# Kernel optimization log

Measured on AMD Instinct MI355X. Metric: run time of the kernel, lower is better.

The kernel has to match this reference:

```python
import jax, jax.numpy as jnp
import numpy as np

NUM_CLASSES = 2
THRESHOLD = 0.35
NEGPOS_RATIO = 3
VAR0, VAR1 = 0.1, 0.2
ALPHA = 1.0
B, P, G = 16, 131072, 64


def _iou(a, b):
    # a: [G,4] point-form gts, b: [P,4] point-form priors -> [G,P]
    tl = jnp.maximum(a[:, None, :2], b[None, :, :2])
    br = jnp.minimum(a[:, None, 2:], b[None, :, 2:])
    wh = jnp.clip(br - tl, 0.0)
    inter = wh[..., 0] * wh[..., 1]
    area_a = (a[:, 2] - a[:, 0]) * (a[:, 3] - a[:, 1])
    area_b = (b[:, 2] - b[:, 0]) * (b[:, 3] - b[:, 1])
    return inter / (area_a[:, None] + area_b[None, :] - inter)


def setup_inputs() -> dict:
    key = jax.random.key(0)
    k1, k2, k3, k4, k5, k6 = jax.random.split(key, 6)
    loc_preds = jax.random.normal(k1, (B, P, 4), jnp.float32)
    cls_preds = jax.random.normal(k2, (B, P, NUM_CLASSES), jnp.float32)
    # priors in center form [cx, cy, w, h]
    pcxy = jax.random.uniform(k3, (P, 2), jnp.float32)
    pwh = 0.02 + 0.15 * jax.random.uniform(k4, (P, 2), jnp.float32)
    priorbox = jnp.concatenate([pcxy, pwh], axis=1)
    # ground-truth boxes; stored as [y1,x1,y2,x2,label] so that the module's
    # column permutation [1,0,3,2] yields valid point-form [x1,y1,x2,y2]
    xy1 = 0.8 * jax.random.uniform(k5, (B, G, 2), jnp.float32)
    wh = 0.02 + 0.1 * jax.random.uniform(k6, (B, G, 2), jnp.float32)
    xy2 = xy1 + wh
    boxes_perm = jnp.stack([xy1[..., 1], xy1[..., 0], xy2[..., 1], xy2[..., 0]], axis=-1)
    labels = jnp.ones((B, G, 1), jnp.float32)  # single foreground class (face)
    targets = jnp.concatenate([boxes_perm, labels], axis=-1)
    return {"loc_preds": loc_preds, "cls_preds": cls_preds,
            "priorbox": priorbox, "targets": targets}


def _loss(loc_preds, cls_preds, priorbox, targets):
    priors_c = priorbox[: loc_preds.shape[1], :]
    priors_pt = jnp.concatenate(
        [priors_c[:, :2] - priors_c[:, 2:] / 2,
         priors_c[:, :2] + priors_c[:, 2:] / 2], axis=1)
    num_g = targets.shape[1]

    def match_one(t):
        gts = t[:, :4][:, jnp.array([1, 0, 3, 2])]  # -> point form [x1,y1,x2,y2]
        labels = t[:, 4]
        ov = _iou(gts, priors_pt)                    # [G,P]
        best_prior_idx = jnp.argmax(ov, axis=1)      # [G]
        bto = jnp.max(ov, axis=0)                    # [P] best gt overlap per prior
        bti = jnp.argmax(ov, axis=0)                 # [P]
        bto = bto.at[best_prior_idx].set(2.0)        # force best prior per gt
        bti = bti.at[best_prior_idx].set(jnp.arange(num_g))
        conf = jnp.where(bto < THRESHOLD, 0.0, labels[bti])
        m = gts[bti]                                 # [P,4] matched gt boxes
        g_cxcy = ((m[:, :2] + m[:, 2:]) / 2 - priors_c[:, :2]) / (VAR0 * priors_c[:, 2:])
        g_wh = jnp.log((m[:, 2:] - m[:, :2]) / priors_c[:, 2:]) / VAR1
        return conf, jnp.concatenate([g_cxcy, g_wh], axis=1)

    cls_batch, loc_batch = jax.vmap(match_one)(targets)
    cls_batch = jax.lax.stop_gradient(cls_batch)   # targets require no grad
    loc_batch = jax.lax.stop_gradient(loc_batch)

    pos = cls_batch > 0                              # [B,P]
    npos = jnp.sum(pos)

    # smooth-L1 over positive priors, mean over selected elements (size_average)
    d = loc_preds - loc_batch
    ad = jnp.abs(d)
    sl1 = jnp.where(ad < 1.0, 0.5 * d * d, ad - 0.5)
    loss_loc = jnp.sum(sl1 * pos[..., None]) / jnp.maximum(npos * 4, 1).astype(sl1.dtype)

    # per-prior CE loss for hard-negative mining
    ignore = cls_batch < 0
    lbl = jnp.where(ignore, 0.0, cls_batch).astype(jnp.int32)
    lse = jax.nn.logsumexp(cls_preds, axis=-1)       # [B,P]
    gathered = jnp.take_along_axis(cls_preds, lbl[..., None], axis=-1)[..., 0]
    loss_c = jnp.where(pos | ignore, 0.0, lse - gathered)
    # two-stage sort: rank of each prior by descending loss
    loss_idx = jnp.argsort(-loss_c, axis=1)
    idx_rank = jnp.argsort(loss_idx, axis=1)
    num_pos_img = jnp.sum(pos, axis=1, keepdims=True)
    num_neg = jnp.minimum(NEGPOS_RATIO * num_pos_img, pos.shape[1] - 1)
    neg = idx_rank < num_neg
    mask = pos | neg
    # cross-entropy over mined samples, mean over selected (size_average)
    loss_cls = jnp.sum((lse - gathered) * mask) / jnp.maximum(jnp.sum(mask), 1).astype(lse.dtype)

    loss = (loss_cls + ALPHA * loss_loc) / npos.astype(lse.dtype)
    return loss, loss_loc, loss_cls


def reference(loc_preds, cls_preds, priorbox, targets):
    return _loss(loc_preds, cls_preds, priorbox, targets)
```

## Files before the change

### kernel.cpp

```cpp
#include <hip/hip_runtime.h>

#define BB 16
#define PP 131072
#define GG 64
#define THRESH 0.35f
#define EXPL 0.086f
#define EXPS 0.0495f
#define CLSB 0.049f
#define NCELL 32
#define NCHM 64
#define CPM 2048
#define NCHL 64
#define CPL 2048
#define NCC 64
#define CPC 2048

#define OFF_BESTP   0
#define OFF_H1TOT   524288
#define OFF_NPOSP   786432
#define OFF_PCP     790528
#define OFF_LOCP    794624
#define OFF_CIDX    798720
#define OFF_NEGS    798784
#define OFF_DONE    798848
#define OFF_RESN    798912
#define OFF_RESK    798976
#define OFF_RESC    799040
#define OFF_RESL    799104
#define OFF_PU8     799168
#define OFF_KEYS    2896320
#define OFF_CAND    11284928

__global__ __launch_bounds__(256) void k_match(
    const float* __restrict__ priorbox, const float* __restrict__ targets,
    unsigned long long* __restrict__ bestp, unsigned char* __restrict__ pu8,
    unsigned* __restrict__ h1tot, unsigned* __restrict__ cidx,
    float* __restrict__ negs, unsigned* __restrict__ done)
{
    __shared__ unsigned mskS[2 * NCELL * NCELL];
    __shared__ unsigned mskL[2 * NCELL * NCELL];
    __shared__ float4 gxy[GG];
    __shared__ unsigned long long sbest[GG];
    const int b = blockIdx.y, chunk = blockIdx.x, tid = threadIdx.x;

    if (tid < 64) h1tot[b * 4096 + chunk * 64 + tid] = 0u;
    if (chunk == 0 && tid == 0) { cidx[b] = 0u; negs[b] = 0.f; if (b == 0) *done = 0u; }
    for (int i = tid; i < 2 * NCELL * NCELL; i += 256) { mskS[i] = 0u; mskL[i] = 0u; }
    if (tid < GG) {
        const float* t = targets + (size_t)(b * GG + tid) * 5;
        gxy[tid] = make_float4(t[1], t[0], t[3], t[2]);
        sbest[tid] = 0ull;
    }
    __syncthreads();

    {
        const int g = tid & 63, strip = tid >> 6;
        float4 a = gxy[g];
        unsigned bit = 1u << (g & 31);
        const int word = g >> 5;
        {
            int cx0 = max(0, (int)((a.x - EXPS) * (float)NCELL));
            int cx1 = min(NCELL - 1, (int)ceilf((a.z + EXPS) * (float)NCELL) - 1);
            int cy0 = max(0, (int)((a.y - EXPS) * (float)NCELL));
            int cy1 = min(NCELL - 1, (int)ceilf((a.w + EXPS) * (float)NCELL) - 1);
            for (int cy = cy0 + strip; cy <= cy1; cy += 4)
                for (int cx = cx0; cx <= cx1; cx++)
                    atomicOr(&mskS[2 * (cy * NCELL + cx) + word], bit);
        }
        {
            int cx0 = max(0, (int)((a.x - EXPL) * (float)NCELL));
            int cx1 = min(NCELL - 1, (int)ceilf((a.z + EXPL) * (float)NCELL) - 1);
            int cy0 = max(0, (int)((a.y - EXPL) * (float)NCELL));
            int cy1 = min(NCELL - 1, (int)ceilf((a.w + EXPL) * (float)NCELL) - 1);
            for (int cy = cy0 + strip; cy <= cy1; cy += 4)
                for (int cx = cx0; cx <= cx1; cx++)
                    atomicOr(&mskL[2 * (cy * NCELL + cx) + word], bit);
        }
    }
    __syncthreads();

#pragma unroll
    for (int j = 0; j < 8; j++) {
        const int p = chunk * CPM + j * 256 + tid;
        float4 pr = *reinterpret_cast<const float4*>(priorbox + (size_t)p * 4);
        float hx = 0.5f * pr.z, hy = 0.5f * pr.w;
        float px1 = pr.x - hx, py1 = pr.y - hy;
        float px2 = pr.x + hx, py2 = pr.y + hy;
        float par = (px2 - px1) * (py2 - py1);
        int cx = min(NCELL - 1, max(0, (int)(pr.x * (float)NCELL)));
        int cy = min(NCELL - 1, max(0, (int)(pr.y * (float)NCELL)));
        const unsigned* mb = (fmaxf(hx, hy) <= CLSB) ? mskS : mskL;
        uint2 mm = *reinterpret_cast<const uint2*>(&mb[2 * (cy * NCELL + cx)]);
        unsigned long long m = ((unsigned long long)mm.y << 32) | mm.x;
        const unsigned long long notp = (unsigned long long)(~(unsigned)p);
        float bv = -1.f; int bg = 0;
        while (m) {
            const int g0 = __ffsll(m) - 1; m &= m - 1;
            const bool has1 = (m != 0ull);
            const int g1 = has1 ? (__ffsll(m) - 1) : g0;
            if (has1) m &= m - 1;
            float4 a0 = gxy[g0];
            float4 a1 = gxy[g1];
            float w0 = fmaxf(fminf(a0.z, px2) - fmaxf(a0.x, px1), 0.f);
            float h0 = fmaxf(fminf(a0.w, py2) - fmaxf(a0.y, py1), 0.f);
            float w1 = fmaxf(fminf(a1.z, px2) - fmaxf(a1.x, px1), 0.f);
            float h1 = fmaxf(fminf(a1.w, py2) - fmaxf(a1.y, py1), 0.f);
            float ar0 = (a0.z - a0.x) * (a0.w - a0.y);
            float ar1 = (a1.z - a1.x) * (a1.w - a1.y);
            float i0 = w0 * h0, i1 = w1 * h1;
            float v0 = i0 * __builtin_amdgcn_rcpf(ar0 + par - i0);
            float v1 = i1 * __builtin_amdgcn_rcpf(ar1 + par - i1);
            if (v0 > bv) { bv = v0; bg = g0; }
            if (has1 && v1 > bv) { bv = v1; bg = g1; }
            if (v0 > 0.f)
                atomicMax(&sbest[g0],
                          (((unsigned long long)__float_as_uint(v0)) << 32) | notp);
            if (has1 && v1 > 0.f)
                atomicMax(&sbest[g1],
                          (((unsigned long long)__float_as_uint(v1)) << 32) | notp);
        }
        pu8[(size_t)b * PP + p] = (unsigned char)(bg | ((bv >= THRESH) ? 0x80 : 0));
    }

    __syncthreads();
    if (tid < GG) bestp[(b * NCHM + chunk) * GG + tid] = sbest[tid];
}

__global__ __launch_bounds__(256) void k_loss(
    const float* __restrict__ loc_preds, const float* __restrict__ cls_preds,
    const float* __restrict__ priorbox, const float* __restrict__ targets,
    const unsigned long long* __restrict__ bestp, const unsigned char* __restrict__ pu8,
    unsigned* __restrict__ keys, unsigned* __restrict__ h1tot,
    int* __restrict__ nposp, float* __restrict__ pcp, float* __restrict__ locp)
{
    __shared__ unsigned hcnt[4096];
    __shared__ unsigned ovr[CPL];
    __shared__ float4 gxy[GG];
    __shared__ float glab[GG];
    __shared__ float sred[8];
    __shared__ int sredi[4];
    const int b = blockIdx.y, chunk = blockIdx.x, tid = threadIdx.x;
    const int lane = tid & 63, wid = tid >> 6;

    for (int i = tid; i < 4096; i += 256) hcnt[i] = 0u;
    for (int i = tid; i < CPL; i += 256) ovr[i] = 0u;
    if (tid < GG) {
        const float* t = targets + (size_t)(b * GG + tid) * 5;
        gxy[tid] = make_float4(t[1], t[0], t[3], t[2]);
        glab[tid] = t[4];
    }
    __syncthreads();
    if (tid < GG) {
        unsigned long long m = 0ull;
#pragma unroll 8
        for (int c = 0; c < NCHM; c++) {
            unsigned long long v = bestp[(b * NCHM + c) * GG + tid];
            m = v > m ? v : m;
        }
        if (m) {
            unsigned p = ~((unsigned)(m & 0xFFFFFFFFull));
            if ((int)(p >> 11) == chunk)
                atomicMax(&ovr[p & (CPL - 1)], (unsigned)tid + 1u);
        }
    }
    __syncthreads();

    float locpart = 0.f, clspart = 0.f; int cnt = 0;
#pragma unroll
    for (int j = 0; j < 8; j++) {
        const int plocal = j * 256 + tid;
        const size_t ip = (size_t)b * PP + chunk * CPL + plocal;
        const unsigned m8 = pu8[ip];
        int g = m8 & 63;
        bool pos = (m8 >> 7) != 0;
        const unsigned o = ovr[plocal];
        if (o) { pos = true; g = (int)o - 1; }
        const float2 cl = *reinterpret_cast<const float2*>(cls_preds + ip * 2);
        const float mx = fmaxf(cl.x, cl.y);
        const float lse = mx + log1pf(expf(fminf(cl.x, cl.y) - mx));
        unsigned key = 0u;
        if (pos && glab[g] > 0.f) {
            float gathered = (((int)glab[g]) == 0) ? cl.x : cl.y;
            clspart += lse - gathered;
            cnt++;
            const int p = chunk * CPL + plocal;
            float4 pr = *reinterpret_cast<const float4*>(priorbox + (size_t)p * 4);
            float4 gt = gxy[g];
            float gcx = ((gt.x + gt.z) * 0.5f - pr.x) / (0.1f * pr.z);
            float gcy = ((gt.y + gt.w) * 0.5f - pr.y) / (0.1f * pr.w);
            float gw = logf((gt.z - gt.x) / pr.z) / 0.2f;
            float gh = logf((gt.w - gt.y) / pr.w) / 0.2f;
            float4 lp = *reinterpret_cast<const float4*>(loc_preds + ip * 4);
            float d0 = lp.x - gcx, d1 = lp.y - gcy, d2 = lp.z - gw, d3 = lp.w - gh;
            float a0 = fabsf(d0), a1 = fabsf(d1), a2 = fabsf(d2), a3 = fabsf(d3);
            locpart += ((a0 < 1.f) ? 0.5f * d0 * d0 : a0 - 0.5f)
                     + ((a1 < 1.f) ? 0.5f * d1 * d1 : a1 - 0.5f)
                     + ((a2 < 1.f) ? 0.5f * d2 * d2 : a2 - 0.5f)
                     + ((a3 < 1.f) ? 0.5f * d3 * d3 : a3 - 0.5f);
        } else {
            float lc = lse - cl.x;
            key = __float_as_uint(lc);
            atomicAdd(&hcnt[key >> 20], 1u);
        }
        keys[ip] = key;
    }

    for (int o = 32; o; o >>= 1) {
        locpart += __shfl_xor(locpart, o);
        clspart += __shfl_xor(clspart, o);
        cnt     += __shfl_xor(cnt, o);
    }
    if (lane == 0) { sred[wid] = locpart; sred[4 + wid] = clspart; sredi[wid] = cnt; }
    __syncthreads();
    if (tid == 0) {
        float l = sred[0] + sred[1] + sred[2] + sred[3];
        float c = sred[4] + sred[5] + sred[6] + sred[7];
        int n = sredi[0] + sredi[1] + sredi[2] + sredi[3];
        nposp[b * NCHL + chunk] = n;
        pcp[b * NCHL + chunk] = c;
        locp[b * NCHL + chunk] = l;
    }
    __syncthreads();
    for (int i = tid; i < 4096; i += 256) {
        unsigned cc = hcnt[i];
        if (cc) atomicAdd(&h1tot[b * 4096 + i], cc);
    }
}

template <int NBINS>
__device__ void find_kth_par(const unsigned* __restrict__ h, int k, int* sel, int* krem)
{
    constexpr int PER = NBINS / 256;
    __shared__ unsigned wsum_[4];
    __shared__ int res_[2];
    const int tid = threadIdx.x, lane = tid & 63, wid = tid >> 6;
    __syncthreads();
    unsigned s = 0;
#pragma unroll
    for (int i = 0; i < PER; i++) s += h[NBINS - 1 - (tid * PER + i)];
    unsigned incl = s;
    for (int d = 1; d < 64; d <<= 1) {
        unsigned t = __shfl_up(incl, d);
        if (lane >= d) incl += t;
    }
    if (lane == 63) wsum_[wid] = incl;
    if (tid == 0) { res_[0] = -1; res_[1] = 0; }
    __syncthreads();
    unsigned woff = 0;
    for (int w = 0; w < 4; w++) woff += (w < wid) ? wsum_[w] : 0u;
    const unsigned texcl = woff + incl - s;
    if (k > 0 && texcl < (unsigned)k && texcl + s >= (unsigned)k) {
        unsigned run = texcl;
        for (int i = 0; i < PER; i++) {
            unsigned hv = h[NBINS - 1 - (tid * PER + i)];
            run += hv;
            if (run >= (unsigned)k) {
                res_[0] = NBINS - 1 - (tid * PER + i);
                res_[1] = k - (int)(run - hv);
                break;
            }
        }
    }
    __syncthreads();
    *sel = res_[0]; *krem = res_[1];
}

__device__ float block_sum_f(float v)
{
    __shared__ float rs[4];
    const int tid = threadIdx.x;
    __syncthreads();
    for (int o = 32; o; o >>= 1) v += __shfl_xor(v, o);
    if ((tid & 63) == 0) rs[tid >> 6] = v;
    __syncthreads();
    return rs[0] + rs[1] + rs[2] + rs[3];
}

__device__ int np_of_image(const int* __restrict__ nposp, int b)
{
    __shared__ int snp;
    const int tid = threadIdx.x;
    int v = (tid < 64) ? nposp[b * NCHL + tid] : 0;
    if (tid < 64) {
        for (int o = 32; o; o >>= 1) v += __shfl_xor(v, o);
        if (tid == 0) snp = v;
    }
    __syncthreads();
    return snp;
}

__global__ __launch_bounds__(256) void k_compact(
    const unsigned* __restrict__ keys, const unsigned* __restrict__ h1tot,
    const int* __restrict__ nposp, unsigned* __restrict__ cand,
    unsigned* __restrict__ cidx, float* __restrict__ negs)
{
    __shared__ unsigned wcnt[4], wbase[4];
    __shared__ unsigned bbase;
    const int b = blockIdx.y, chunk = blockIdx.x, tid = threadIdx.x;
    const int lane = tid & 63, wid = tid >> 6;

    unsigned kv[8];
#pragma unroll
    for (int j = 0; j < 8; j++)
        kv[j] = keys[(size_t)b * PP + chunk * CPC + j * 256 + tid];

    const int np = np_of_image(nposp, b);
    const int k = min(3 * np, PP - 1);
    int sel1, kk1;
    find_kth_par<4096>(h1tot + b * 4096, k, &sel1, &kk1);
    const unsigned s1 = (unsigned)sel1;

    float nv = 0.f;
    if (sel1 >= 0) {
#pragma unroll
        for (int j = 0; j < 8; j++)
            if ((kv[j] >> 20) > s1) nv += __uint_as_float(kv[j]);
    }
    float nsum = block_sum_f(nv);
    if (tid == 0 && nsum != 0.f) atomicAdd(&negs[b], nsum);

    unsigned long long mv[8];
    unsigned wn = 0;
#pragma unroll
    for (int j = 0; j < 8; j++) {
        mv[j] = __ballot((kv[j] >> 20) == s1);
        wn += (unsigned)__popcll(mv[j]);
    }
    if (lane == 0) wcnt[wid] = wn;
    __syncthreads();
    if (tid == 0) {
        unsigned run = 0;
        for (int w = 0; w < 4; w++) { wbase[w] = run; run += wcnt[w]; }
        bbase = run ? atomicAdd(&cidx[b], run) : 0u;
    }
    __syncthreads();
    unsigned run = bbase + wbase[wid];
    const unsigned long long lanemask = (1ull << lane) - 1ull;
#pragma unroll
    for (int j = 0; j < 8; j++) {
        if ((kv[j] >> 20) == s1)
            cand[(size_t)b * PP + run + (unsigned)__popcll(mv[j] & lanemask)] = kv[j];
        run += (unsigned)__popcll(mv[j]);
    }
}

__global__ __launch_bounds__(256) void k_select(
    const unsigned* __restrict__ cand, const unsigned* __restrict__ cidx,
    const unsigned* __restrict__ h1tot, const int* __restrict__ nposp,
    const float* __restrict__ pcp, const float* __restrict__ locp,
    const float* __restrict__ negs,
    int* __restrict__ resn, int* __restrict__ resk,
    float* __restrict__ resc, float* __restrict__ resl,
    unsigned* __restrict__ done, float* __restrict__ out)
{
    __shared__ unsigned ch[1024];
    __shared__ float cs[1024];
    __shared__ int lastflag;
    const int b = blockIdx.x, tid = threadIdx.x;

    const int np = np_of_image(nposp, b);
    const int k = min(3 * np, PP - 1);
    int sel1, kk1;
    find_kth_par<4096>(h1tot + b * 4096, k, &sel1, &kk1);
    const unsigned ncand = cidx[b];

    float pv = (tid < 64) ? pcp[b * NCHL + tid] : 0.f;
    float lv = (tid < 64) ? locp[b * NCHL + tid] : 0.f;
    float pcsum = block_sum_f(pv);
    float locsum = block_sum_f(lv);

    for (int i = tid; i < 1024; i += 256) { ch[i] = 0u; cs[i] = 0.f; }
    __syncthreads();
    for (unsigned i = tid; i < ncand; i += 256) {
        unsigned v = cand[(size_t)b * PP + i];
        unsigned bin = (v >> 10) & 1023u;
        atomicAdd(&ch[bin], 1u);
        atomicAdd(&cs[bin], __uint_as_float(v));
    }
    __syncthreads();
    int sel2, kk2;
    find_kth_par<1024>(ch, (sel1 < 0) ? 0 : kk1, &sel2, &kk2);
    float s2v = 0.f;
    for (int i = tid * 4; i < tid * 4 + 4; i++)
        if (sel2 >= 0 && i > sel2) s2v += cs[i];
    float sumhi2 = block_sum_f(s2v);

    __syncthreads();
    for (int i = tid; i < 1024; i += 256) { ch[i] = 0u; cs[i] = 0.f; }
    __syncthreads();
    if (sel2 >= 0) {
        for (unsigned i = tid; i < ncand; i += 256) {
            unsigned v = cand[(size_t)b * PP + i];
            if (((v >> 10) & 1023u) == (unsigned)sel2) {
                atomicAdd(&ch[v & 1023u], 1u);
                atomicAdd(&cs[v & 1023u], __uint_as_float(v));
            }
        }
    }
    __syncthreads();
    int sel3, needeq;
    find_kth_par<1024>(ch, (sel2 < 0) ? 0 : kk2, &sel3, &needeq);
    float s3v = 0.f;
    for (int i = tid * 4; i < tid * 4 + 4; i++)
        if (sel3 >= 0 && i > sel3) s3v += cs[i];
    float sumhi3 = block_sum_f(s3v);

    if (tid == 0) {
        float add = 0.f;
        if (sel3 >= 0 && needeq > 0) {
            unsigned Kstar = ((unsigned)sel1 << 20) | ((unsigned)sel2 << 10) | (unsigned)sel3;
            add = needeq * __uint_as_float(Kstar);
        }
        resn[b] = np;
        resk[b] = k;
        resc[b] = pcsum + negs[b] + sumhi2 + sumhi3 + add;
        resl[b] = locsum;
        __threadfence();
        lastflag = (atomicAdd(done, 1u) == BB - 1) ? 1 : 0;
    }
    __syncthreads();
    if (!lastflag) return;
    if (tid == 0) __threadfence();
    __syncthreads();

    int n = 0, kk = 0; float c = 0.f, l = 0.f;
    if (tid < BB) { n = resn[tid]; kk = resk[tid]; c = resc[tid]; l = resl[tid]; }
    if (tid < 64) {
        for (int o = 8; o; o >>= 1) {
            n += __shfl_xor(n, o); kk += __shfl_xor(kk, o);
            c += __shfl_xor(c, o); l += __shfl_xor(l, o);
        }
    }
    if (tid == 0) {
        long long maskc = (long long)n + kk;
        float denom_loc = (float)((4 * n > 1) ? 4 * n : 1);
        float denom_cls = (float)((maskc > 1) ? maskc : 1);
        float loss_loc = l / denom_loc;
        float loss_cls = c / denom_cls;
        out[0] = (loss_cls + loss_loc) / (float)n;
        out[1] = loss_loc;
        out[2] = loss_cls;
    }
}

extern "C" void kernel_launch(void* const* d_in, const int* in_sizes, int n_in,
                              void* d_out, int out_size, void* d_ws, size_t ws_size,
                              hipStream_t stream)
{
    const float* loc_preds = (const float*)d_in[0];
    const float* cls_preds = (const float*)d_in[1];
    const float* priorbox  = (const float*)d_in[2];
    const float* targets   = (const float*)d_in[3];
    float* out = (float*)d_out;

    char* ws = (char*)d_ws;
    unsigned long long* bestp = (unsigned long long*)(ws + OFF_BESTP);
    unsigned* h1tot = (unsigned*)(ws + OFF_H1TOT);
    int*      nposp = (int*)(ws + OFF_NPOSP);
    float*    pcp   = (float*)(ws + OFF_PCP);
    float*    locp  = (float*)(ws + OFF_LOCP);
    unsigned* cidx  = (unsigned*)(ws + OFF_CIDX);
    float*    negs  = (float*)(ws + OFF_NEGS);
    unsigned* done  = (unsigned*)(ws + OFF_DONE);
    int*      resn  = (int*)(ws + OFF_RESN);
    int*      resk  = (int*)(ws + OFF_RESK);
    float*    resc  = (float*)(ws + OFF_RESC);
    float*    resl  = (float*)(ws + OFF_RESL);
    unsigned char* pu8 = (unsigned char*)(ws + OFF_PU8);
    unsigned* keys  = (unsigned*)(ws + OFF_KEYS);
    unsigned* cand  = (unsigned*)(ws + OFF_CAND);

    k_match<<<dim3(NCHM, BB), 256, 0, stream>>>(priorbox, targets, bestp, pu8,
                                                h1tot, cidx, negs, done);
    k_loss<<<dim3(NCHL, BB), 256, 0, stream>>>(loc_preds, cls_preds, priorbox, targets,
                                               bestp, pu8, keys, h1tot,
                                               nposp, pcp, locp);
    k_compact<<<dim3(NCC, BB), 256, 0, stream>>>(keys, h1tot, nposp, cand, cidx, negs);
    k_select<<<BB, 256, 0, stream>>>(cand, cidx, h1tot, nposp, pcp, locp, negs,
                                     resn, resk, resc, resl, done, out);
}
```

Measured before the change: 99.50 us.

## Fuse matching and loss kernels, patch forced-match priors in a small fix kernel

Merges the prior-matching pass and the per-prior loss/key pass into one kernel. Each block now computes loss contributions right after matching, using the threshold-based assignment. The per-gt forced best-prior overrides are applied afterwards by a tiny k_fix kernel, which adjusts keys, histogram counts and partial sums incrementally. A separate zeroing kernel replaces the in-kernel initialization. This removes one full pass over pu8/priorbox and a kernel launch, at the cost of extra correction logic that must exactly reproduce the override semantics.

```diff
diff --git a/kernel.cpp b/kernel.cpp
--- a/kernel.cpp
+++ b/kernel.cpp
@@ -8,10 +8,8 @@
 #define EXPS 0.0495f
 #define CLSB 0.049f
 #define NCELL 32
-#define NCHM 64
-#define CPM 2048
-#define NCHL 64
-#define CPL 2048
+#define NCH 64
+#define CPR 2048
 #define NCC 64
 #define CPC 2048
 
@@ -31,24 +29,42 @@
 #define OFF_KEYS    2896320
 #define OFF_CAND    11284928
 
-__global__ __launch_bounds__(256) void k_match(
-    const float* __restrict__ priorbox, const float* __restrict__ targets,
-    unsigned long long* __restrict__ bestp, unsigned char* __restrict__ pu8,
+__global__ __launch_bounds__(256) void k_zero(
     unsigned* __restrict__ h1tot, unsigned* __restrict__ cidx,
     float* __restrict__ negs, unsigned* __restrict__ done)
 {
+    const int gid = blockIdx.x * 256 + threadIdx.x;
+    h1tot[gid] = 0u;
+    if (blockIdx.x == 0) {
+        if (threadIdx.x < BB) { cidx[threadIdx.x] = 0u; negs[threadIdx.x] = 0.f; }
+        if (threadIdx.x == BB) *done = 0u;
+    }
+}
+
+__global__ __launch_bounds__(256) void k_matchloss(
+    const float* __restrict__ priorbox, const float* __restrict__ targets,
+    const float* __restrict__ loc_preds, const float* __restrict__ cls_preds,
+    unsigned long long* __restrict__ bestp, unsigned char* __restrict__ pu8,
+    unsigned* __restrict__ keys, unsigned* __restrict__ h1tot,
+    int* __restrict__ nposp, float* __restrict__ pcp, float* __restrict__ locp)
+{
     __shared__ unsigned mskS[2 * NCELL * NCELL];
     __shared__ unsigned mskL[2 * NCELL * NCELL];
+    __shared__ unsigned hcnt[4096];
     __shared__ float4 gxy[GG];
+    __shared__ float glab[GG];
     __shared__ unsigned long long sbest[GG];
+    __shared__ float sred[8];
+    __shared__ int sredi[4];
     const int b = blockIdx.y, chunk = blockIdx.x, tid = threadIdx.x;
-
-    if (tid < 64) h1tot[b * 4096 + chunk * 64 + tid] = 0u;
-    if (chunk == 0 && tid == 0) { cidx[b] = 0u; negs[b] = 0.f; if (b == 0) *done = 0u; }
+    const int lane = tid & 63, wid = tid >> 6;
+
     for (int i = tid; i < 2 * NCELL * NCELL; i += 256) { mskS[i] = 0u; mskL[i] = 0u; }
+    for (int i = tid; i < 4096; i += 256) hcnt[i] = 0u;
     if (tid < GG) {
         const float* t = targets + (size_t)(b * GG + tid) * 5;
         gxy[tid] = make_float4(t[1], t[0], t[3], t[2]);
+        glab[tid] = t[4];
         sbest[tid] = 0ull;
     }
     __syncthreads();
@@ -79,9 +95,11 @@
     }
     __syncthreads();
 
+    float locpart = 0.f, clspart = 0.f; int cnt = 0;
 #pragma unroll
     for (int j = 0; j < 8; j++) {
-        const int p = chunk * CPM + j * 256 + tid;
+        const int p = chunk * CPR + j * 256 + tid;
+        const size_t ip = (size_t)b * PP + p;
         float4 pr = *reinterpret_cast<const float4*>(priorbox + (size_t)p * 4);
         float hx = 0.5f * pr.z, hy = 0.5f * pr.w;
         float px1 = pr.x - hx, py1 = pr.y - hy;
@@ -119,73 +137,18 @@
                 atomicMax(&sbest[g1],
                           (((unsigned long long)__float_as_uint(v1)) << 32) | notp);
         }
-        pu8[(size_t)b * PP + p] = (unsigned char)(bg | ((bv >= THRESH) ? 0x80 : 0));
-    }
-
-    __syncthreads();
-    if (tid < GG) bestp[(b * NCHM + chunk) * GG + tid] = sbest[tid];
-}
-
-__global__ __launch_bounds__(256) void k_loss(
-    const float* __restrict__ loc_preds, const float* __restrict__ cls_preds,
-    const float* __restrict__ priorbox, const float* __restrict__ targets,
-    const unsigned long long* __restrict__ bestp, const unsigned char* __restrict__ pu8,
-    unsigned* __restrict__ keys, unsigned* __restrict__ h1tot,
-    int* __restrict__ nposp, float* __restrict__ pcp, float* __restrict__ locp)
-{
-    __shared__ unsigned hcnt[4096];
-    __shared__ unsigned ovr[CPL];
-    __shared__ float4 gxy[GG];
-    __shared__ float glab[GG];
-    __shared__ float sred[8];
-    __shared__ int sredi[4];
-    const int b = blockIdx.y, chunk = blockIdx.x, tid = threadIdx.x;
-    const int lane = tid & 63, wid = tid >> 6;
-
-    for (int i = tid; i < 4096; i += 256) hcnt[i] = 0u;
-    for (int i = tid; i < CPL; i += 256) ovr[i] = 0u;
-    if (tid < GG) {
-        const float* t = targets + (size_t)(b * GG + tid) * 5;
-        gxy[tid] = make_float4(t[1], t[0], t[3], t[2]);
-        glab[tid] = t[4];
-    }
-    __syncthreads();
-    if (tid < GG) {
-        unsigned long long m = 0ull;
-#pragma unroll 8
-        for (int c = 0; c < NCHM; c++) {
-            unsigned long long v = bestp[(b * NCHM + c) * GG + tid];
-            m = v > m ? v : m;
-        }
-        if (m) {
-            unsigned p = ~((unsigned)(m & 0xFFFFFFFFull));
-            if ((int)(p >> 11) == chunk)
-                atomicMax(&ovr[p & (CPL - 1)], (unsigned)tid + 1u);
-        }
-    }
-    __syncthreads();
-
-    float locpart = 0.f, clspart = 0.f; int cnt = 0;
-#pragma unroll
-    for (int j = 0; j < 8; j++) {
-        const int plocal = j * 256 + tid;
-        const size_t ip = (size_t)b * PP + chunk * CPL + plocal;
-        const unsigned m8 = pu8[ip];
-        int g = m8 & 63;
-        bool pos = (m8 >> 7) != 0;
-        const unsigned o = ovr[plocal];
-        if (o) { pos = true; g = (int)o - 1; }
+        const bool posbit = (bv >= THRESH);
+        pu8[ip] = (unsigned char)(bg | (posbit ? 0x80 : 0));
+
         const float2 cl = *reinterpret_cast<const float2*>(cls_preds + ip * 2);
         const float mx = fmaxf(cl.x, cl.y);
         const float lse = mx + log1pf(expf(fminf(cl.x, cl.y) - mx));
         unsigned key = 0u;
-        if (pos && glab[g] > 0.f) {
-            float gathered = (((int)glab[g]) == 0) ? cl.x : cl.y;
+        if (posbit && glab[bg] > 0.f) {
+            float gathered = (((int)glab[bg]) == 0) ? cl.x : cl.y;
             clspart += lse - gathered;
             cnt++;
-            const int p = chunk * CPL + plocal;
-            float4 pr = *reinterpret_cast<const float4*>(priorbox + (size_t)p * 4);
-            float4 gt = gxy[g];
+            float4 gt = gxy[bg];
             float gcx = ((gt.x + gt.z) * 0.5f - pr.x) / (0.1f * pr.z);
             float gcy = ((gt.y + gt.w) * 0.5f - pr.y) / (0.1f * pr.w);
             float gw = logf((gt.z - gt.x) / pr.z) / 0.2f;
@@ -213,17 +176,111 @@
     if (lane == 0) { sred[wid] = locpart; sred[4 + wid] = clspart; sredi[wid] = cnt; }
     __syncthreads();
     if (tid == 0) {
-        float l = sred[0] + sred[1] + sred[2] + sred[3];
-        float c = sred[4] + sred[5] + sred[6] + sred[7];
-        int n = sredi[0] + sredi[1] + sredi[2] + sredi[3];
-        nposp[b * NCHL + chunk] = n;
-        pcp[b * NCHL + chunk] = c;
-        locp[b * NCHL + chunk] = l;
-    }
+        nposp[b * NCH + chunk] = sredi[0] + sredi[1] + sredi[2] + sredi[3];
+        pcp[b * NCH + chunk] = sred[4] + sred[5] + sred[6] + sred[7];
+        locp[b * NCH + chunk] = sred[0] + sred[1] + sred[2] + sred[3];
+    }
+    if (tid < GG) bestp[(b * NCH + chunk) * GG + tid] = sbest[tid];
     __syncthreads();
     for (int i = tid; i < 4096; i += 256) {
         unsigned cc = hcnt[i];
         if (cc) atomicAdd(&h1tot[b * 4096 + i], cc);
+    }
+}
+
+__global__ void k_fix(
+    const float* __restrict__ priorbox, const float* __restrict__ targets,
+    const float* __restrict__ loc_preds, const float* __restrict__ cls_preds,
+    const unsigned long long* __restrict__ bestp, const unsigned char* __restrict__ pu8,
+    unsigned* __restrict__ keys, unsigned* __restrict__ h1tot,
+    int* __restrict__ nposp, float* __restrict__ pcp, float* __restrict__ locp)
+{
+    __shared__ unsigned sp[GG];
+    const int b = blockIdx.x, g = threadIdx.x;
+
+    unsigned long long m = 0ull;
+#pragma unroll 8
+    for (int c = 0; c < NCH; c++) {
+        unsigned long long v = bestp[(b * NCH + c) * GG + g];
+        m = v > m ? v : m;
+    }
+    sp[g] = m ? ~((unsigned)(m & 0xFFFFFFFFull)) : 0xFFFFFFFFu;
+    __syncthreads();
+
+    bool winner = (sp[g] != 0xFFFFFFFFu);
+    if (winner)
+        for (int g2 = g + 1; g2 < GG; g2++)
+            if (sp[g2] == sp[g]) { winner = false; break; }
+
+    int dn = 0; float dpc = 0.f, dloc = 0.f;
+    if (winner) {
+        const unsigned p = sp[g];
+        const size_t ip = (size_t)b * PP + p;
+        const unsigned m8 = pu8[ip];
+        const int oldg = m8 & 63;
+        const bool oldposbit = (m8 >> 7) != 0;
+        const float labg = targets[(size_t)(b * GG + g) * 5 + 4];
+        const float labold = targets[(size_t)(b * GG + oldg) * 5 + 4];
+        const bool counted_old = oldposbit && (labold > 0.f);
+        const bool counted_new = (labg > 0.f);
+        const float2 cl = *reinterpret_cast<const float2*>(cls_preds + ip * 2);
+        const float mx = fmaxf(cl.x, cl.y);
+        const float lse = mx + log1pf(expf(fminf(cl.x, cl.y) - mx));
+        float4 pr = *reinterpret_cast<const float4*>(priorbox + (size_t)p * 4);
+        float4 lp = *reinterpret_cast<const float4*>(loc_preds + ip * 4);
+
+#define SL1(GT)                                                             \
+        ({                                                                  \
+            const float* t_ = targets + (size_t)(b * GG + (GT)) * 5;        \
+            float x1 = t_[1], y1 = t_[0], x2 = t_[3], y2 = t_[2];           \
+            float gcx = ((x1 + x2) * 0.5f - pr.x) / (0.1f * pr.z);          \
+            float gcy = ((y1 + y2) * 0.5f - pr.y) / (0.1f * pr.w);          \
+            float gw = logf((x2 - x1) / pr.z) / 0.2f;                       \
+            float gh = logf((y2 - y1) / pr.w) / 0.2f;                       \
+            float d0 = lp.x - gcx, d1 = lp.y - gcy, d2 = lp.z - gw,         \
+                  d3 = lp.w - gh;                                           \
+            float a0 = fabsf(d0), a1 = fabsf(d1), a2 = fabsf(d2),           \
+                  a3 = fabsf(d3);                                           \
+            ((a0 < 1.f) ? 0.5f * d0 * d0 : a0 - 0.5f) +                     \
+            ((a1 < 1.f) ? 0.5f * d1 * d1 : a1 - 0.5f) +                     \
+            ((a2 < 1.f) ? 0.5f * d2 * d2 : a2 - 0.5f) +                     \
+            ((a3 < 1.f) ? 0.5f * d3 * d3 : a3 - 0.5f);                      \
+        })
+
+        if (counted_new) {
+            float gathered = (((int)labg) == 0) ? cl.x : cl.y;
+            if (!counted_old) {
+                unsigned okey = keys[ip];
+                if (okey) atomicSub(&h1tot[b * 4096 + (okey >> 20)], 1u);
+                keys[ip] = 0u;
+                dn = 1; dpc = lse - gathered; dloc = SL1(g);
+            } else {
+                float gathold = (((int)labold) == 0) ? cl.x : cl.y;
+                dpc = gathold - gathered;
+                dloc = SL1(g) - SL1(oldg);
+            }
+        } else {
+            if (counted_old) {
+                float gathold = (((int)labold) == 0) ? cl.x : cl.y;
+                dn = -1; dpc = -(lse - gathold); dloc = -SL1(oldg);
+                float lc = lse - cl.x;
+                unsigned nk = __float_as_uint(lc);
+                keys[ip] = nk;
+                atomicAdd(&h1tot[b * 4096 + (nk >> 20)], 1u);
+            }
+        }
+#undef SL1
+    }
+
+    for (int o = 32; o; o >>= 1) {
+        dn += __shfl_xor(dn, o);
+        dpc += __shfl_xor(dpc, o);
+        dloc += __shfl_xor(dloc, o);
+    }
+    if (g == 0) {
+        if (dn)         atomicAdd(&nposp[b * NCH], dn);
+        if (dpc != 0.f) atomicAdd(&pcp[b * NCH], dpc);
+        if (dloc != 0.f) atomicAdd(&locp[b * NCH], dloc);
     }
 }
 
@@ -280,7 +337,7 @@
 {
     __shared__ int snp;
     const int tid = threadIdx.x;
-    int v = (tid < 64) ? nposp[b * NCHL + tid] : 0;
+    int v = (tid < 64) ? nposp[b * NCH + tid] : 0;
     if (tid < 64) {
         for (int o = 32; o; o >>= 1) v += __shfl_xor(v, o);
         if (tid == 0) snp = v;
@@ -364,8 +421,8 @@
     find_kth_par<4096>(h1tot + b * 4096, k, &sel1, &kk1);
     const unsigned ncand = cidx[b];
 
-    float pv = (tid < 64) ? pcp[b * NCHL + tid] : 0.f;
-    float lv = (tid < 64) ? locp[b * NCHL + tid] : 0.f;
+    float pv = (tid < 64) ? pcp[b * NCH + tid] : 0.f;
+    float lv = (tid < 64) ? locp[b * NCH + tid] : 0.f;
     float pcsum = block_sum_f(pv);
     float locsum = block_sum_f(lv);
 
@@ -470,11 +527,12 @@
     unsigned* keys  = (unsigned*)(ws + OFF_KEYS);
     unsigned* cand  = (unsigned*)(ws + OFF_CAND);
 
-    k_match<<<dim3(NCHM, BB), 256, 0, stream>>>(priorbox, targets, bestp, pu8,
-                                                h1tot, cidx, negs, done);
-    k_loss<<<dim3(NCHL, BB), 256, 0, stream>>>(loc_preds, cls_preds, priorbox, targets,
-                                               bestp, pu8, keys, h1tot,
-                                               nposp, pcp, locp);
+    k_zero<<<256, 256, 0, stream>>>(h1tot, cidx, negs, done);
+    k_matchloss<<<dim3(NCH, BB), 256, 0, stream>>>(priorbox, targets, loc_preds,
+                                                   cls_preds, bestp, pu8, keys, h1tot,
+                                                   nposp, pcp, locp);
+    k_fix<<<BB, 64, 0, stream>>>(priorbox, targets, loc_preds, cls_preds,
+                                 bestp, pu8, keys, h1tot, nposp, pcp, locp);
     k_compact<<<dim3(NCC, BB), 256, 0, stream>>>(keys, h1tot, nposp, cand, cidx, negs);
     k_select<<<BB, 256, 0, stream>>>(cand, cidx, h1tot, nposp, pcp, locp, negs,
                                      resn, resk, resc, resl, done, out);
```

After: 109.0 us. 1.09x slower.

## Sort priors by spatial cell and size class before matching to cut divergence

Applied to the files above, without the earlier changes.

Two new kernels build a counting sort of priors by grid cell and size class: a per-block histogram, then a prefix scan and a scatter into an order array. The match kernel then walks priors in that order, so threads in a wavefront share the same candidate ground-truth mask and loop trip count, which reduces divergence in the IoU loop. The cost is two extra launches plus gathered prior loads and scattered byte stores of pu8. The sort is recomputed on every call, and the best-prior tie-break still uses the original prior index.

```diff
diff --git a/kernel.cpp b/kernel.cpp
--- a/kernel.cpp
+++ b/kernel.cpp
@@ -8,10 +8,10 @@
 #define EXPS 0.0495f
 #define CLSB 0.049f
 #define NCELL 32
-#define NCHM 64
-#define CPM 2048
-#define NCHL 64
-#define CPL 2048
+#define NBKT 2048
+#define NSB 64
+#define NCH 64
+#define CPR 2048
 #define NCC 64
 #define CPC 2048
 
@@ -30,9 +30,84 @@
 #define OFF_PU8     799168
 #define OFF_KEYS    2896320
 #define OFF_CAND    11284928
+#define OFF_ORDER   19673536
+#define OFF_PCOUNT  20197824
+
+__device__ __forceinline__ int prior_bucket(float4 pr)
+{
+    int cx = min(NCELL - 1, max(0, (int)(pr.x * (float)NCELL)));
+    int cy = min(NCELL - 1, max(0, (int)(pr.y * (float)NCELL)));
+    int cls = (fmaxf(0.5f * pr.z, 0.5f * pr.w) <= CLSB) ? 0 : 1;
+    return (cy * NCELL + cx) * 2 + cls;
+}
+
+__global__ __launch_bounds__(256) void k_scount(
+    const float* __restrict__ priorbox, unsigned* __restrict__ pcount)
+{
+    __shared__ unsigned h[NBKT];
+    const int blk = blockIdx.x, tid = threadIdx.x;
+    for (int i = tid; i < NBKT; i += 256) h[i] = 0u;
+    __syncthreads();
+#pragma unroll
+    for (int j = 0; j < 8; j++) {
+        const int q = blk * 2048 + j * 256 + tid;
+        float4 pr = *reinterpret_cast<const float4*>(priorbox + (size_t)q * 4);
+        atomicAdd(&h[prior_bucket(pr)], 1u);
+    }
+    __syncthreads();
+    for (int i = tid; i < NBKT; i += 256) pcount[blk * NBKT + i] = h[i];
+}
+
+__global__ __launch_bounds__(256) void k_scatter(
+    const float* __restrict__ priorbox, const unsigned* __restrict__ pcount,
+    unsigned* __restrict__ order)
+{
+    __shared__ unsigned sbase[NBKT];
+    __shared__ unsigned wsum[4];
+    const int blk = blockIdx.x, tid = threadIdx.x;
+    const int lane = tid & 63, wid = tid >> 6;
+
+    unsigned tot[8], cb[8];
+    unsigned tsum = 0;
+#pragma unroll
+    for (int i = 0; i < 8; i++) {
+        const int c = tid * 8 + i;
+        unsigned t = 0, before = 0;
+        for (int b2 = 0; b2 < NSB; b2++) {
+            unsigned v = pcount[b2 * NBKT + c];
+            t += v;
+            before += (b2 < blk) ? v : 0u;
+        }
+        tot[i] = t; cb[i] = before; tsum += t;
+    }
+    unsigned incl = tsum;
+    for (int d = 1; d < 64; d <<= 1) {
+        unsigned t = __shfl_up(incl, d);
+        if (lane >= d) incl += t;
+    }
+    if (lane == 63) wsum[wid] = incl;
+    __syncthreads();
+    unsigned woff = 0;
+    for (int w = 0; w < 4; w++) woff += (w < wid) ? wsum[w] : 0u;
+    unsigned run = woff + incl - tsum;
+#pragma unroll
+    for (int i = 0; i < 8; i++) {
+        sbase[tid * 8 + i] = run + cb[i];
+        run += tot[i];
+    }
+    __syncthreads();
+#pragma unroll
+    for (int j = 0; j < 8; j++) {
+        const int q = blk * 2048 + j * 256 + tid;
+        float4 pr = *reinterpret_cast<const float4*>(priorbox + (size_t)q * 4);
+        unsigned slot = atomicAdd(&sbase[prior_bucket(pr)], 1u);
+        order[slot] = (unsigned)q;
+    }
+}
 
 __global__ __launch_bounds__(256) void k_match(
     const float* __restrict__ priorbox, const float* __restrict__ targets,
+    const unsigned* __restrict__ order,
     unsigned long long* __restrict__ bestp, unsigned char* __restrict__ pu8,
     unsigned* __restrict__ h1tot, unsigned* __restrict__ cidx,
     float* __restrict__ negs, unsigned* __restrict__ done)
@@ -81,8 +156,9 @@
 
 #pragma unroll
     for (int j = 0; j < 8; j++) {
-        const int p = chunk * CPM + j * 256 + tid;
-        float4 pr = *reinterpret_cast<const float4*>(priorbox + (size_t)p * 4);
+        const int s = chunk * CPR + j * 256 + tid;
+        const unsigned q = order[s];
+        float4 pr = *reinterpret_cast<const float4*>(priorbox + (size_t)q * 4);
         float hx = 0.5f * pr.z, hy = 0.5f * pr.w;
         float px1 = pr.x - hx, py1 = pr.y - hy;
         float px2 = pr.x + hx, py2 = pr.y + hy;
@@ -92,7 +168,7 @@
         const unsigned* mb = (fmaxf(hx, hy) <= CLSB) ? mskS : mskL;
         uint2 mm = *reinterpret_cast<const uint2*>(&mb[2 * (cy * NCELL + cx)]);
         unsigned long long m = ((unsigned long long)mm.y << 32) | mm.x;
-        const unsigned long long notp = (unsigned long long)(~(unsigned)p);
+        const unsigned long long notp = (unsigned long long)(~q);
         float bv = -1.f; int bg = 0;
         while (m) {
             const int g0 = __ffsll(m) - 1; m &= m - 1;
@@ -119,11 +195,11 @@
                 atomicMax(&sbest[g1],
                           (((unsigned long long)__float_as_uint(v1)) << 32) | notp);
         }
-        pu8[(size_t)b * PP + p] = (unsigned char)(bg | ((bv >= THRESH) ? 0x80 : 0));
-    }
-
-    __syncthreads();
-    if (tid < GG) bestp[(b * NCHM + chunk) * GG + tid] = sbest[tid];
+        pu8[(size_t)b * PP + q] = (unsigned char)(bg | ((bv >= THRESH) ? 0x80 : 0));
+    }
+
+    __syncthreads();
+    if (tid < GG) bestp[(b * NCH + chunk) * GG + tid] = sbest[tid];
 }
 
 __global__ __launch_bounds__(256) void k_loss(
@@ -134,7 +210,7 @@
     int* __restrict__ nposp, float* __restrict__ pcp, float* __restrict__ locp)
 {
     __shared__ unsigned hcnt[4096];
-    __shared__ unsigned ovr[CPL];
+    __shared__ unsigned ovr[CPR];
     __shared__ float4 gxy[GG];
     __shared__ float glab[GG];
     __shared__ float sred[8];
@@ -143,7 +219,7 @@
     const int lane = tid & 63, wid = tid >> 6;
 
     for (int i = tid; i < 4096; i += 256) hcnt[i] = 0u;
-    for (int i = tid; i < CPL; i += 256) ovr[i] = 0u;
+    for (int i = tid; i < CPR; i += 256) ovr[i] = 0u;
     if (tid < GG) {
         const float* t = targets + (size_t)(b * GG + tid) * 5;
         gxy[tid] = make_float4(t[1], t[0], t[3], t[2]);
@@ -153,14 +229,14 @@
     if (tid < GG) {
         unsigned long long m = 0ull;
 #pragma unroll 8
-        for (int c = 0; c < NCHM; c++) {
-            unsigned long long v = bestp[(b * NCHM + c) * GG + tid];
+        for (int c = 0; c < NCH; c++) {
+            unsigned long long v = bestp[(b * NCH + c) * GG + tid];
             m = v > m ? v : m;
         }
         if (m) {
             unsigned p = ~((unsigned)(m & 0xFFFFFFFFull));
             if ((int)(p >> 11) == chunk)
-                atomicMax(&ovr[p & (CPL - 1)], (unsigned)tid + 1u);
+                atomicMax(&ovr[p & (CPR - 1)], (unsigned)tid + 1u);
         }
     }
     __syncthreads();
@@ -169,7 +245,7 @@
 #pragma unroll
     for (int j = 0; j < 8; j++) {
         const int plocal = j * 256 + tid;
-        const size_t ip = (size_t)b * PP + chunk * CPL + plocal;
+        const size_t ip = (size_t)b * PP + chunk * CPR + plocal;
         const unsigned m8 = pu8[ip];
         int g = m8 & 63;
         bool pos = (m8 >> 7) != 0;
@@ -183,7 +259,7 @@
             float gathered = (((int)glab[g]) == 0) ? cl.x : cl.y;
             clspart += lse - gathered;
             cnt++;
-            const int p = chunk * CPL + plocal;
+            const int p = chunk * CPR + plocal;
             float4 pr = *reinterpret_cast<const float4*>(priorbox + (size_t)p * 4);
             float4 gt = gxy[g];
             float gcx = ((gt.x + gt.z) * 0.5f - pr.x) / (0.1f * pr.z);
@@ -213,12 +289,9 @@
     if (lane == 0) { sred[wid] = locpart; sred[4 + wid] = clspart; sredi[wid] = cnt; }
     __syncthreads();
     if (tid == 0) {
-        float l = sred[0] + sred[1] + sred[2] + sred[3];
-        float c = sred[4] + sred[5] + sred[6] + sred[7];
-        int n = sredi[0] + sredi[1] + sredi[2] + sredi[3];
-        nposp[b * NCHL + chunk] = n;
-        pcp[b * NCHL + chunk] = c;
-        locp[b * NCHL + chunk] = l;
+        nposp[b * NCH + chunk] = sredi[0] + sredi[1] + sredi[2] + sredi[3];
+        pcp[b * NCH + chunk] = sred[4] + sred[5] + sred[6] + sred[7];
+        locp[b * NCH + chunk] = sred[0] + sred[1] + sred[2] + sred[3];
     }
     __syncthreads();
     for (int i = tid; i < 4096; i += 256) {
@@ -280,7 +353,7 @@
 {
     __shared__ int snp;
     const int tid = threadIdx.x;
-    int v = (tid < 64) ? nposp[b * NCHL + tid] : 0;
+    int v = (tid < 64) ? nposp[b * NCH + tid] : 0;
     if (tid < 64) {
         for (int o = 32; o; o >>= 1) v += __shfl_xor(v, o);
         if (tid == 0) snp = v;
@@ -364,8 +437,8 @@
     find_kth_par<4096>(h1tot + b * 4096, k, &sel1, &kk1);
     const unsigned ncand = cidx[b];
 
-    float pv = (tid < 64) ? pcp[b * NCHL + tid] : 0.f;
-    float lv = (tid < 64) ? locp[b * NCHL + tid] : 0.f;
+    float pv = (tid < 64) ? pcp[b * NCH + tid] : 0.f;
+    float lv = (tid < 64) ? locp[b * NCH + tid] : 0.f;
     float pcsum = block_sum_f(pv);
     float locsum = block_sum_f(lv);
 
@@ -469,12 +542,16 @@
     unsigned char* pu8 = (unsigned char*)(ws + OFF_PU8);
     unsigned* keys  = (unsigned*)(ws + OFF_KEYS);
     unsigned* cand  = (unsigned*)(ws + OFF_CAND);
-
-    k_match<<<dim3(NCHM, BB), 256, 0, stream>>>(priorbox, targets, bestp, pu8,
-                                                h1tot, cidx, negs, done);
-    k_loss<<<dim3(NCHL, BB), 256, 0, stream>>>(loc_preds, cls_preds, priorbox, targets,
-                                               bestp, pu8, keys, h1tot,
-                                               nposp, pcp, locp);
+    unsigned* order = (unsigned*)(ws + OFF_ORDER);
+    unsigned* pcount= (unsigned*)(ws + OFF_PCOUNT);
+
+    k_scount<<<NSB, 256, 0, stream>>>(priorbox, pcount);
+    k_scatter<<<NSB, 256, 0, stream>>>(priorbox, pcount, order);
+    k_match<<<dim3(NCH, BB), 256, 0, stream>>>(priorbox, targets, order, bestp, pu8,
+                                               h1tot, cidx, negs, done);
+    k_loss<<<dim3(NCH, BB), 256, 0, stream>>>(loc_preds, cls_preds, priorbox, targets,
+                                              bestp, pu8, keys, h1tot,
+                                              nposp, pcp, locp);
     k_compact<<<dim3(NCC, BB), 256, 0, stream>>>(keys, h1tot, nposp, cand, cidx, negs);
     k_select<<<BB, 256, 0, stream>>>(cand, cidx, h1tot, nposp, pcp, locp, negs,
                                      resn, resk, resc, resl, done, out);
```

After: 171.5 us. +72.4%, slower.
